# Performance work log

Measured on AMD Instinct MI355X. Metric: run time of the kernel, lower is better.

Reference implementation:

```python
import jax, jax.numpy as jnp
import numpy as np

B, H, W = 256, 512, 512
H_SCALE, W_SCALE = 16, 16
FWHM_THRESHOLD = 0.5


def setup_inputs() -> dict:
    key = jax.random.key(0)
    k1, k2 = jax.random.split(key)
    output = jax.random.normal(k1, (B, H, W), dtype=jnp.float32)
    target = jax.random.uniform(k2, (B, H, W), dtype=jnp.float32)
    return {"output": output, "target": target}


def _ramp(idx, lo, L):
    # Symmetric 1->10->1 ramp over window [lo, lo+L), matching
    # torch.cat([linspace(1,10,(L+1)//2), flip(...)]) semantics:
    # value at offset j equals linspace(1,10,n)[min(j, L-1-j)], n=(L+1)//2.
    j = idx - lo                      # offset into window
    n = (L + 1) // 2
    k = jnp.minimum(j, L - 1 - j)
    denom = jnp.maximum(n - 1, 1).astype(jnp.float32)  # linspace(1,10,1)==[1]
    val = 1.0 + 9.0 * k.astype(jnp.float32) / denom
    inside = (j >= 0) & (j < L)
    return val, inside


def _penalty_weight(target):
    b, h, w = target.shape
    flat = target.reshape(b, h * w)
    max_pos = jnp.argmax(flat, axis=1)   # first max, like torch.max
    max_val = jnp.max(flat, axis=1)
    ph = max_pos // w
    pw = max_pos % w
    dh, dw = h // H_SCALE, w // W_SCALE
    top = jnp.maximum(ph - dh, 0)
    bot = jnp.minimum(ph + dh, h)
    left = jnp.maximum(pw - dw, 0)
    right = jnp.minimum(pw + dw, w)
    rows = jnp.arange(h)
    cols = jnp.arange(w)
    vh, inh = jax.vmap(lambda lo, L: _ramp(rows, lo, L))(top, bot - top)        # [b,h]
    vw, inw = jax.vmap(lambda lo, L: _ramp(cols, lo, L))(left, right - left)    # [b,w]
    inside = inh[:, :, None] & inw[:, None, :]                                  # [b,h,w]
    active = (max_val >= FWHM_THRESHOLD)[:, None, None]
    return jnp.where(inside & active, vh[:, :, None] * vw[:, None, :], 1.0)


def reference(output, target):
    pen = _penalty_weight(target)
    return jnp.mean((output - target) ** 2 * pen)
```

## Files before the change

kernel.cpp:

```cpp
#include <hip/hip_runtime.h>
#include <stdint.h>

#define NB   256
#define HH   512
#define WW   512
#define HWSZ (HH * WW)
#define SPLIT 16
#define THREADS 256


__global__ __launch_bounds__(THREADS) void pass1_kernel(
    const float* __restrict__ outp, const float* __restrict__ tgt,
    unsigned long long* __restrict__ keys, double* __restrict__ acc) {
  const int blk   = blockIdx.x;
  const int b     = blk / SPLIT;
  const int chunk = blk % SPLIT;
  const int f4_per_block = HWSZ / 4 / SPLIT;
  const size_t base4 = (size_t)b * (HWSZ / 4) + (size_t)chunk * f4_per_block;
  const float4* o4 = (const float4*)outp + base4;
  const float4* t4 = (const float4*)tgt  + base4;

  const int t = threadIdx.x;
  float    sum     = 0.0f;
  float    bestv   = -1.0f;
  unsigned bestidx = 0u;

  #pragma unroll
  for (int i = 0; i < f4_per_block / THREADS; ++i) {
    const int p = i * THREADS + t;
    const float4 ov = o4[p];
    const float4 tv = t4[p];
    const float d0 = ov.x - tv.x, d1 = ov.y - tv.y;
    const float d2 = ov.z - tv.z, d3 = ov.w - tv.w;
    sum += d0 * d0 + d1 * d1 + d2 * d2 + d3 * d3;
    const unsigned fi = (unsigned)((chunk * f4_per_block + p) * 4);
    if (tv.x > bestv) { bestv = tv.x; bestidx = fi;     }
    if (tv.y > bestv) { bestv = tv.y; bestidx = fi + 1; }
    if (tv.z > bestv) { bestv = tv.z; bestidx = fi + 2; }
    if (tv.w > bestv) { bestv = tv.w; bestidx = fi + 3; }
  }

  unsigned long long key =
      ((unsigned long long)__float_as_uint(bestv) << 32) | (unsigned long long)(~bestidx);

  const int lane = t & 63, wave = t >> 6;
  #pragma unroll
  for (int off = 32; off > 0; off >>= 1) {
    unsigned long long ok = __shfl_down(key, off, 64);
    if (ok > key) key = ok;
    sum += __shfl_down(sum, off, 64);
  }
  __shared__ unsigned long long skey[THREADS / 64];
  __shared__ float              ssum[THREADS / 64];
  if (lane == 0) { skey[wave] = key; ssum[wave] = sum; }
  __syncthreads();
  if (t == 0) {
    unsigned long long k = skey[0];
    float s = ssum[0];
    #pragma unroll
    for (int i = 1; i < THREADS / 64; ++i) {
      if (skey[i] > k) k = skey[i];
      s += ssum[i];
    }
    atomicMax(&keys[b], k);
    atomicAdd(acc, (double)s);
  }
}

__global__ __launch_bounds__(THREADS) void pass2_kernel(
    const float* __restrict__ outp, const float* __restrict__ tgt,
    const unsigned long long* __restrict__ keys, double* __restrict__ acc) {
  const int b = blockIdx.x;
  const unsigned long long key = keys[b];
  const float maxv = __uint_as_float((unsigned)(key >> 32));
  if (maxv < 0.5f) return;
  const unsigned idx = ~(unsigned)(key & 0xFFFFFFFFull);
  const int ph = (int)(idx / WW), pw = (int)(idx % WW);
  const int dh = HH / 16, dw = WW / 16;
  const int top  = max(ph - dh, 0), bot   = min(ph + dh, HH);
  const int left = max(pw - dw, 0), right = min(pw + dw, WW);
  const int Lh = bot - top, Lw = right - left;
  const float nh = (float)max((Lh + 1) / 2 - 1, 1);
  const float nw = (float)max((Lw + 1) / 2 - 1, 1);
  const float* ob = outp + (size_t)b * HWSZ;
  const float* tb = tgt  + (size_t)b * HWSZ;

  float sum = 0.0f;
  const int n_elems = Lh * Lw;
  for (int j = threadIdx.x; j < n_elems; j += THREADS) {
    const int r = j / Lw, c = j % Lw;
    const int kr = min(r, Lh - 1 - r), kc = min(c, Lw - 1 - c);
    const float vh = 1.0f + 9.0f * (float)kr / nh;
    const float vw = 1.0f + 9.0f * (float)kc / nw;
    const int row = top + r, col = left + c;
    const float d = ob[row * WW + col] - tb[row * WW + col];
    sum += (vh * vw - 1.0f) * d * d;
  }

  const int lane = threadIdx.x & 63, wave = threadIdx.x >> 6;
  #pragma unroll
  for (int off = 32; off > 0; off >>= 1) sum += __shfl_down(sum, off, 64);
  __shared__ float ssum[THREADS / 64];
  if (lane == 0) ssum[wave] = sum;
  __syncthreads();
  if (threadIdx.x == 0) {
    float s = 0.0f;
    #pragma unroll
    for (int i = 0; i < THREADS / 64; ++i) s += ssum[i];
    atomicAdd(acc, (double)s);
  }
}

__global__ void finalize_kernel(const double* __restrict__ acc, float* __restrict__ out) {
  out[0] = (float)(acc[0] / (double)((size_t)NB * HWSZ));
}

extern "C" void kernel_launch(void* const* d_in, const int* in_sizes, int n_in,
                              void* d_out, int out_size, void* d_ws, size_t ws_size,
                              hipStream_t stream) {
  const float* outp = (const float*)d_in[0];
  const float* tgt  = (const float*)d_in[1];
  unsigned long long* keys = (unsigned long long*)d_ws;
  double* acc = (double*)((char*)d_ws + NB * sizeof(unsigned long long));

  hipMemsetAsync(d_ws, 0, NB * sizeof(unsigned long long) + sizeof(double), stream);

  pass1_kernel<<<NB * SPLIT, THREADS, 0, stream>>>(outp, tgt, keys, acc);
  pass2_kernel<<<NB, THREADS, 0, stream>>>(outp, tgt, keys, acc);
  finalize_kernel<<<1, 1, 0, stream>>>(acc, (float*)d_out);
}
```

Measured before the change: 517.9 us.

## Fuse pass1, pass2 and finalize into one kernel via last-block-per-batch counters

Merges the three kernels into one launch. A per-batch atomic counter marks the last chunk block of each batch, and that block computes the windowed penalty correction once the max key is final. A global done counter lets the final block write the mean. This removes two kernel launches and the serialization gap between passes, and lets the correction reads hit cache while still warm. In exchange it adds atomics and fences, and the correction work is spread unevenly across the tail blocks.

```diff
diff --git a/kernel.cpp b/kernel.cpp
--- a/kernel.cpp
+++ b/kernel.cpp
@@ -1,22 +1,45 @@
 #include <hip/hip_runtime.h>
 #include <stdint.h>
 
-#define NB   256
-#define HH   512
-#define WW   512
-#define HWSZ (HH * WW)
-#define SPLIT 16
+#define NB      256
+#define HH      512
+#define WW      512
+#define HWSZ    (HH * WW)
+#define SPLIT   16
 #define THREADS 256
+#define F4_PER_BLOCK (HWSZ / 4 / SPLIT)
+#define ITERS        (F4_PER_BLOCK / THREADS)
 
+struct Ws {
+  unsigned long long keys[NB];
+  int                cnt[NB];
+  int                done;
+  int                pad;
+  double             acc;
+};
 
-__global__ __launch_bounds__(THREADS) void pass1_kernel(
+__device__ __forceinline__ float block_reduce_sum(float v, float* lds) {
+  const int lane = threadIdx.x & 63, wave = threadIdx.x >> 6;
+  #pragma unroll
+  for (int off = 32; off > 0; off >>= 1) v += __shfl_down(v, off, 64);
+  if (lane == 0) lds[wave] = v;
+  __syncthreads();
+  float s = 0.0f;
+  if (threadIdx.x == 0) {
+    #pragma unroll
+    for (int i = 0; i < THREADS / 64; ++i) s += lds[i];
+  }
+  __syncthreads();
+  return s;
+}
+
+__global__ __launch_bounds__(THREADS) void fused_kernel(
     const float* __restrict__ outp, const float* __restrict__ tgt,
-    unsigned long long* __restrict__ keys, double* __restrict__ acc) {
+    Ws* __restrict__ ws, float* __restrict__ out) {
   const int blk   = blockIdx.x;
-  const int b     = blk / SPLIT;
-  const int chunk = blk % SPLIT;
-  const int f4_per_block = HWSZ / 4 / SPLIT;
-  const size_t base4 = (size_t)b * (HWSZ / 4) + (size_t)chunk * f4_per_block;
+  const int b     = blk >> 4;
+  const int chunk = blk & (SPLIT - 1);
+  const size_t base4 = (size_t)b * (HWSZ / 4) + (size_t)chunk * F4_PER_BLOCK;
   const float4* o4 = (const float4*)outp + base4;
   const float4* t4 = (const float4*)tgt  + base4;
 
@@ -26,14 +49,14 @@
   unsigned bestidx = 0u;
 
   #pragma unroll
-  for (int i = 0; i < f4_per_block / THREADS; ++i) {
+  for (int i = 0; i < ITERS; ++i) {
     const int p = i * THREADS + t;
     const float4 ov = o4[p];
     const float4 tv = t4[p];
     const float d0 = ov.x - tv.x, d1 = ov.y - tv.y;
     const float d2 = ov.z - tv.z, d3 = ov.w - tv.w;
     sum += d0 * d0 + d1 * d1 + d2 * d2 + d3 * d3;
-    const unsigned fi = (unsigned)((chunk * f4_per_block + p) * 4);
+    const unsigned fi = (unsigned)((chunk * F4_PER_BLOCK + p) * 4);
     if (tv.x > bestv) { bestv = tv.x; bestidx = fi;     }
     if (tv.y > bestv) { bestv = tv.y; bestidx = fi + 1; }
     if (tv.z > bestv) { bestv = tv.z; bestidx = fi + 2; }
@@ -43,6 +66,11 @@
   unsigned long long key =
       ((unsigned long long)__float_as_uint(bestv) << 32) | (unsigned long long)(~bestidx);
 
+  __shared__ float              s_sum[THREADS / 64];
+  __shared__ unsigned long long s_keys[THREADS / 64];
+  __shared__ int                s_last;
+  __shared__ unsigned long long s_key;
+
   const int lane = t & 63, wave = t >> 6;
   #pragma unroll
   for (int off = 32; off > 0; off >>= 1) {
@@ -50,69 +78,67 @@
     if (ok > key) key = ok;
     sum += __shfl_down(sum, off, 64);
   }
-  __shared__ unsigned long long skey[THREADS / 64];
-  __shared__ float              ssum[THREADS / 64];
-  if (lane == 0) { skey[wave] = key; ssum[wave] = sum; }
+  if (lane == 0) { s_keys[wave] = key; s_sum[wave] = sum; }
   __syncthreads();
+
   if (t == 0) {
-    unsigned long long k = skey[0];
-    float s = ssum[0];
+    unsigned long long k = s_keys[0];
+    float s = s_sum[0];
     #pragma unroll
     for (int i = 1; i < THREADS / 64; ++i) {
-      if (skey[i] > k) k = skey[i];
-      s += ssum[i];
+      if (s_keys[i] > k) k = s_keys[i];
+      s += s_sum[i];
     }
-    atomicMax(&keys[b], k);
-    atomicAdd(acc, (double)s);
+    atomicMax(&ws->keys[b], k);
+    atomicAdd(&ws->acc, (double)s);
+    __threadfence();
+    s_last = atomicAdd(&ws->cnt[b], 1);
   }
-}
+  __syncthreads();
 
-__global__ __launch_bounds__(THREADS) void pass2_kernel(
-    const float* __restrict__ outp, const float* __restrict__ tgt,
-    const unsigned long long* __restrict__ keys, double* __restrict__ acc) {
-  const int b = blockIdx.x;
-  const unsigned long long key = keys[b];
-  const float maxv = __uint_as_float((unsigned)(key >> 32));
-  if (maxv < 0.5f) return;
-  const unsigned idx = ~(unsigned)(key & 0xFFFFFFFFull);
-  const int ph = (int)(idx / WW), pw = (int)(idx % WW);
-  const int dh = HH / 16, dw = WW / 16;
-  const int top  = max(ph - dh, 0), bot   = min(ph + dh, HH);
-  const int left = max(pw - dw, 0), right = min(pw + dw, WW);
-  const int Lh = bot - top, Lw = right - left;
-  const float nh = (float)max((Lh + 1) / 2 - 1, 1);
-  const float nw = (float)max((Lw + 1) / 2 - 1, 1);
-  const float* ob = outp + (size_t)b * HWSZ;
-  const float* tb = tgt  + (size_t)b * HWSZ;
+  if (s_last != SPLIT - 1) return;
 
-  float sum = 0.0f;
-  const int n_elems = Lh * Lw;
-  for (int j = threadIdx.x; j < n_elems; j += THREADS) {
-    const int r = j / Lw, c = j % Lw;
-    const int kr = min(r, Lh - 1 - r), kc = min(c, Lw - 1 - c);
-    const float vh = 1.0f + 9.0f * (float)kr / nh;
-    const float vw = 1.0f + 9.0f * (float)kc / nw;
-    const int row = top + r, col = left + c;
-    const float d = ob[row * WW + col] - tb[row * WW + col];
-    sum += (vh * vw - 1.0f) * d * d;
+  __threadfence();
+  if (t == 0) s_key = atomicMax(&ws->keys[b], 0ull);
+  __syncthreads();
+  const unsigned long long k = s_key;
+  const float maxv = __uint_as_float((unsigned)(k >> 32));
+
+  float corr = 0.0f;
+  if (maxv >= 0.5f) {
+    const unsigned idx = ~(unsigned)(k & 0xFFFFFFFFull);
+    const int ph = (int)(idx / WW), pw = (int)(idx % WW);
+    const int dh = HH / 16, dw = WW / 16;
+    const int top  = max(ph - dh, 0), bot   = min(ph + dh, HH);
+    const int left = max(pw - dw, 0), right = min(pw + dw, WW);
+    const int Lh = bot - top, Lw = right - left;
+    const float nh = (float)max((Lh + 1) / 2 - 1, 1);
+    const float nw = (float)max((Lw + 1) / 2 - 1, 1);
+    const float* ob = outp + (size_t)b * HWSZ;
+    const float* tb = tgt  + (size_t)b * HWSZ;
+    const int n_elems = Lh * Lw;
+    for (int j = t; j < n_elems; j += THREADS) {
+      const int r = j / Lw, c = j % Lw;
+      const int kr = min(r, Lh - 1 - r), kc = min(c, Lw - 1 - c);
+      const float vh = 1.0f + 9.0f * (float)kr / nh;
+      const float vw = 1.0f + 9.0f * (float)kc / nw;
+      const int row = top + r, col = left + c;
+      const float d = ob[row * WW + col] - tb[row * WW + col];
+      corr += (vh * vw - 1.0f) * d * d;
+    }
   }
+  const float corr_total = block_reduce_sum(corr, s_sum);
 
-  const int lane = threadIdx.x & 63, wave = threadIdx.x >> 6;
-  #pragma unroll
-  for (int off = 32; off > 0; off >>= 1) sum += __shfl_down(sum, off, 64);
-  __shared__ float ssum[THREADS / 64];
-  if (lane == 0) ssum[wave] = sum;
-  __syncthreads();
-  if (threadIdx.x == 0) {
-    float s = 0.0f;
-    #pragma unroll
-    for (int i = 0; i < THREADS / 64; ++i) s += ssum[i];
-    atomicAdd(acc, (double)s);
+  if (t == 0) {
+    atomicAdd(&ws->acc, (double)corr_total);
+    __threadfence();
+    const int d = atomicAdd(&ws->done, 1);
+    if (d == NB - 1) {
+      __threadfence();
+      const double total = atomicAdd(&ws->acc, 0.0);
+      out[0] = (float)(total / (double)((size_t)NB * HWSZ));
+    }
   }
-}
-
-__global__ void finalize_kernel(const double* __restrict__ acc, float* __restrict__ out) {
-  out[0] = (float)(acc[0] / (double)((size_t)NB * HWSZ));
 }
 
 extern "C" void kernel_launch(void* const* d_in, const int* in_sizes, int n_in,
@@ -120,12 +146,9 @@
                               hipStream_t stream) {
   const float* outp = (const float*)d_in[0];
   const float* tgt  = (const float*)d_in[1];
-  unsigned long long* keys = (unsigned long long*)d_ws;
-  double* acc = (double*)((char*)d_ws + NB * sizeof(unsigned long long));
+  Ws* ws = (Ws*)d_ws;
 
-  hipMemsetAsync(d_ws, 0, NB * sizeof(unsigned long long) + sizeof(double), stream);
+  hipMemsetAsync(d_ws, 0, sizeof(Ws), stream);
 
-  pass1_kernel<<<NB * SPLIT, THREADS, 0, stream>>>(outp, tgt, keys, acc);
-  pass2_kernel<<<NB, THREADS, 0, stream>>>(outp, tgt, keys, acc);
-  finalize_kernel<<<1, 1, 0, stream>>>(acc, (float*)d_out);
+  fused_kernel<<<NB * SPLIT, THREADS, 0, stream>>>(outp, tgt, ws, (float*)d_out);
 }
```

New measurement: 978.9 us. +89.0%, slower.
